# Kernel tuning notes

Measured on AMD Instinct MI355X. Metric: run time of the kernel, lower is better.

## Reference

```python
import jax, jax.numpy as jnp
import numpy as np

N = 100000        # nodes
E = 1600000       # edges (before self-loops)
F_IN = 128        # input feature dim
HID = 32          # hidden_channels
HEADS = 2
HC = HID * HEADS  # 64, per-conv output width (concat=True)
OUT = 40          # out_channels
NEG_SLOPE = 0.2   # PyG GATConv leaky_relu slope
BN_EPS = 1e-5


def setup_inputs() -> dict:
    key = jax.random.key(0)
    ks = jax.random.split(key, 16)
    g = lambda k, shape, s: jax.random.normal(k, shape, jnp.float32) * s
    node_feat = jax.random.normal(ks[0], (N, F_IN), jnp.float32)
    edge_index = jax.random.randint(ks[1], (2, E), 0, N, jnp.int32)
    inp = {
        "node_feat": node_feat,
        "edge_index": edge_index,
        "W1": g(ks[2], (F_IN, HC), 1.0 / np.sqrt(F_IN)),
        "a_src1": g(ks[3], (HEADS, HID), 0.1),
        "a_dst1": g(ks[4], (HEADS, HID), 0.1),
        "b1": jnp.zeros((HC,), jnp.float32),
        # BatchNorm1d(64) in eval mode (running stats)
        "bn_gamma": jnp.ones((HC,), jnp.float32),
        "bn_beta": jnp.zeros((HC,), jnp.float32),
        "bn_mean": g(ks[5], (HC,), 0.1),
        "bn_var": jax.random.uniform(ks[6], (HC,), jnp.float32, 0.5, 1.5),
        "W2": g(ks[7], (HC, HC), 1.0 / np.sqrt(HC)),
        "a_src2": g(ks[8], (HEADS, HID), 0.1),
        "a_dst2": g(ks[9], (HEADS, HID), 0.1),
        "b2": jnp.zeros((HC,), jnp.float32),
        # final projection 64 -> 40
        "Wf": g(ks[10], (HC, OUT), 1.0 / np.sqrt(HC)),
        "bf": jnp.zeros((OUT,), jnp.float32),
    }
    return inp


def _gat_layer(x, src, dst, W, a_s, a_d, b):
    # x: [N, Fin] -> h: [N, H, C]
    h = (x @ W).reshape(N, HEADS, HID)
    alpha_src = jnp.einsum('nhc,hc->nh', h, a_s)   # [N, H]
    alpha_dst = jnp.einsum('nhc,hc->nh', h, a_d)   # [N, H]
    e = jax.nn.leaky_relu(alpha_src[src] + alpha_dst[dst], NEG_SLOPE)  # [Etot, H]
    m = jax.lax.stop_gradient(jax.ops.segment_max(e, dst, num_segments=N))
    ex = jnp.exp(e - m[dst])
    denom = jax.ops.segment_sum(ex, dst, num_segments=N)
    alpha = ex / (denom[dst] + 1e-16)              # softmax over incoming edges
    msg = h[src] * alpha[:, :, None]               # [Etot, H, C]
    out = jax.ops.segment_sum(msg, dst, num_segments=N)  # [N, H, C]
    return out.reshape(N, HC) + b


def reference(node_feat, edge_index, W1, a_src1, a_dst1, b1,
              bn_gamma, bn_beta, bn_mean, bn_var,
              W2, a_src2, a_dst2, b2, Wf, bf):
    # add self-loops (PyG GATConv default add_self_loops=True)
    loop = jnp.arange(N, dtype=edge_index.dtype)
    src = jnp.concatenate([edge_index[0], loop])
    dst = jnp.concatenate([edge_index[1], loop])

    x1 = _gat_layer(node_feat, src, dst, W1, a_src1, a_dst1, b1)
    # BatchNorm1d eval + ELU (dropout is identity in eval)
    x1 = (x1 - bn_mean) * (bn_gamma / jnp.sqrt(bn_var + BN_EPS)) + bn_beta
    x1 = jax.nn.elu(x1)

    x2 = _gat_layer(x1, src, dst, W2, a_src2, a_dst2, b2)

    # JumpingKnowledge 'max': elementwise max over layer outputs
    xj = jnp.maximum(x1, x2)
    return xj @ Wf + bf
```

## Files before the change

### kernel.cpp

```cpp
#include <hip/hip_runtime.h>
#include <hip/hip_bf16.h>

#define N_NODES 100000
#define E_EDGES 1600000
#define ETOT    1700000
#define NB_SCAN 391
#define EQ4     400000
#define NB_EQ4  1563
#define F_IN    128
#define HC      64
#define OUT_C   40
#define NEG_SLOPE 0.2f
#define BN_EPS  1e-5f

#define P_W1   0
#define P_AS1  8192
#define P_AD1  8256
#define P_B1   8320
#define P_BNG  8384
#define P_BNB  8448
#define P_BNM  8512
#define P_BNV  8576
#define P_W2   8640
#define P_AS2  12736
#define P_AD2  12800
#define P_B2   12864
#define P_WF   12928
#define P_BF   15488
#define P_TOT  15528

typedef __attribute__((ext_vector_type(8))) short short8;
typedef __attribute__((ext_vector_type(4))) float floatx4;
typedef __attribute__((ext_vector_type(4))) unsigned int uintx4;

__device__ __forceinline__ unsigned short f2bf(float f) {
    unsigned int u = __float_as_uint(f);
    unsigned int r = u + 0x7FFFu + ((u >> 16) & 1u);
    return (unsigned short)(r >> 16);
}

__global__ __launch_bounds__(64) void detect_kernel(const unsigned short* __restrict__ x,
                                                    int* __restrict__ flag) {
    int t = threadIdx.x;
    bool huge = false;
#pragma unroll
    for (int i = 0; i < 4; ++i) {
        unsigned short u = x[(t * 4 + i) * 2];
        float v = __uint_as_float(((unsigned int)u) << 16);
        if (!(fabsf(v) < 1e4f)) huge = true;
    }
    unsigned long long b = __ballot(huge);
    if (t == 0) *flag = (b != 0ull) ? 1 : 0;
}

struct CvtArgs { const void* ptr[14]; int len[14]; };

__global__ __launch_bounds__(256) void cvt_params_kernel(CvtArgs a,
                                                         const int* __restrict__ flag,
                                                         float* __restrict__ dst) {
    int f = *flag;
    int i = blockIdx.x * 256 + threadIdx.x;
    if (i >= P_TOT) return;
    int k = 0, off = 0;
    while (i >= off + a.len[k]) { off += a.len[k]; ++k; }
    int j = i - off;
    float v = f ? ((const float*)a.ptr[k])[j]
                : __bfloat162float(((const __hip_bfloat16*)a.ptr[k])[j]);
    dst[i] = v;
}

__global__ __launch_bounds__(256) void build_frags_kernel(const float* __restrict__ prm,
                                                          unsigned short* __restrict__ fw1,
                                                          unsigned short* __restrict__ fw2) {
    int i = blockIdx.x * 256 + threadIdx.x;
    if (i < 8192) {
        int j = i & 7, l = (i >> 3) & 63, q = (i >> 9) & 3, t = i >> 11;
        int k = q * 32 + (l >> 4) * 8 + j;
        int n = t * 16 + (l & 15);
        fw1[i] = f2bf(prm[P_W1 + k * 64 + n]);
    } else if (i < 12288) {
        int f = i - 8192;
        int j = f & 7, l = (f >> 3) & 63, q = (f >> 9) & 1, t = f >> 10;
        int k = q * 32 + (l >> 4) * 8 + j;
        int n = t * 16 + (l & 15);
        fw2[f] = f2bf(prm[P_W2 + k * 64 + n]);
    }
}

__global__ __launch_bounds__(256) void histrank_kernel(const int* __restrict__ ei,
                                                       int* __restrict__ deg,
                                                       int4* __restrict__ rank4) {
    int i4 = blockIdx.x * 256 + threadIdx.x;
    if (i4 >= EQ4) return;
    const unsigned long long* dst2 = (const unsigned long long*)(ei + E_EDGES);
    unsigned long long p0 = __builtin_nontemporal_load(&dst2[i4 * 2]);
    unsigned long long p1 = __builtin_nontemporal_load(&dst2[i4 * 2 + 1]);
    int d0 = (int)(p0 & 0xFFFFFFFFull), d1 = (int)(p0 >> 32);
    int d2 = (int)(p1 & 0xFFFFFFFFull), d3 = (int)(p1 >> 32);
    int4 r;
    r.x = atomicAdd(&deg[d0], 1);
    r.y = atomicAdd(&deg[d1], 1);
    r.z = atomicAdd(&deg[d2], 1);
    r.w = atomicAdd(&deg[d3], 1);
    rank4[i4] = r;
}

__global__ __launch_bounds__(256) void scanA_kernel(const int* __restrict__ deg,
                                                    int* __restrict__ bsum) {
    __shared__ int sm[256];
    int t = threadIdx.x;
    int i = blockIdx.x * 256 + t;
    sm[t] = (i < N_NODES) ? deg[i] + 1 : 0;
    __syncthreads();
    for (int off = 128; off > 0; off >>= 1) {
        if (t < off) sm[t] += sm[t + off];
        __syncthreads();
    }
    if (t == 0) bsum[blockIdx.x] = sm[0];
}

__global__ __launch_bounds__(512) void scanB_kernel(const int* __restrict__ bsum,
                                                    int* __restrict__ boff,
                                                    int* __restrict__ row_start) {
    __shared__ int sm[512];
    int t = threadIdx.x;
    int v = (t < NB_SCAN) ? bsum[t] : 0;
    sm[t] = v;
    __syncthreads();
    for (int off = 1; off < 512; off <<= 1) {
        int o = (t >= off) ? sm[t - off] : 0;
        __syncthreads();
        sm[t] += o;
        __syncthreads();
    }
    if (t < NB_SCAN) boff[t] = sm[t] - v;
    if (t == NB_SCAN - 1) row_start[N_NODES] = sm[t];
}

__global__ __launch_bounds__(256) void scanC_kernel(const int* __restrict__ deg,
                                                    const int* __restrict__ boff,
                                                    int* __restrict__ row_start,
                                                    int* __restrict__ col) {
    __shared__ int sm[256];
    int t = threadIdx.x;
    int i = blockIdx.x * 256 + t;
    int v = (i < N_NODES) ? deg[i] + 1 : 0;
    sm[t] = v;
    __syncthreads();
    for (int off = 1; off < 256; off <<= 1) {
        int o = (t >= off) ? sm[t - off] : 0;
        __syncthreads();
        sm[t] += o;
        __syncthreads();
    }
    if (i < N_NODES) {
        int excl = sm[t] - v + boff[blockIdx.x];
        row_start[i] = excl;
        col[excl]    = i;
    }
}

__global__ __launch_bounds__(256) void scatter_kernel(const int* __restrict__ ei,
                                                      const int4* __restrict__ rank4,
                                                      const int* __restrict__ row_start,
                                                      int* __restrict__ col) {
    int i4 = blockIdx.x * 256 + threadIdx.x;
    if (i4 >= EQ4) return;
    const unsigned long long* dst2 = (const unsigned long long*)(ei + E_EDGES);
    const unsigned long long* src2 = (const unsigned long long*)ei;
    unsigned long long p0 = __builtin_nontemporal_load(&dst2[i4 * 2]);
    unsigned long long p1 = __builtin_nontemporal_load(&dst2[i4 * 2 + 1]);
    unsigned long long q0 = __builtin_nontemporal_load(&src2[i4 * 2]);
    unsigned long long q1 = __builtin_nontemporal_load(&src2[i4 * 2 + 1]);
    int4 r = rank4[i4];
    int d0 = (int)(p0 & 0xFFFFFFFFull), d1 = (int)(p0 >> 32);
    int d2 = (int)(p1 & 0xFFFFFFFFull), d3 = (int)(p1 >> 32);
    int s0 = (int)(q0 & 0xFFFFFFFFull), s1 = (int)(q0 >> 32);
    int s2 = (int)(q1 & 0xFFFFFFFFull), s3 = (int)(q1 >> 32);
    int b0 = row_start[d0];
    int b1 = row_start[d1];
    int b2 = row_start[d2];
    int b3 = row_start[d3];
    col[b0 + 1 + r.x] = s0;
    col[b1 + 1 + r.y] = s1;
    col[b2 + 1 + r.z] = s2;
    col[b3 + 1 + r.w] = s3;
}

__device__ __forceinline__ float leaky(float v) { return v > 0.f ? v : NEG_SLOPE * v; }

__device__ __forceinline__ float red64(float v) {
#pragma unroll
    for (int off = 32; off > 0; off >>= 1) v += __shfl_xor(v, off, 64);
    return v;
}
__device__ __forceinline__ float red16(float v) {
#pragma unroll
    for (int off = 8; off > 0; off >>= 1) v += __shfl_xor(v, off, 64);
    return v;
}

__global__ __launch_bounds__(128) void gemm1_kernel(const void* __restrict__ x,
                                                    const unsigned short* __restrict__ fw1,
                                                    const float* __restrict__ prm,
                                                    const int* __restrict__ flag,
                                                    unsigned short* __restrict__ h_bf,
                                                    float* __restrict__ as_,
                                                    float* __restrict__ ad_) {
    __shared__ short lx[2 * 4 * 64 * 8];
    int t = threadIdx.x;
    int f = *flag;
    int base = blockIdx.x * 32;

#pragma unroll
    for (int i = 0; i < 4; ++i) {
        int cid = i * 128 + t;
        int m = cid >> 4, c = cid & 15;
        int q = c >> 2, g = c & 3;
        int loff = (((m >> 4) * 4 + q) * 64 + g * 16 + (m & 15)) * 8;
        short8 s;
        if (f) {
            const float4* p = (const float4*)((const float*)x + ((size_t)(base + m) << 7) + (c << 3));
            float4 u0 = p[0], u1 = p[1];
            s[0] = (short)f2bf(u0.x); s[1] = (short)f2bf(u0.y);
            s[2] = (short)f2bf(u0.z); s[3] = (short)f2bf(u0.w);
            s[4] = (short)f2bf(u1.x); s[5] = (short)f2bf(u1.y);
            s[6] = (short)f2bf(u1.z); s[7] = (short)f2bf(u1.w);
        } else {
            s = *(const short8*)((const unsigned short*)x + ((size_t)(base + m) << 7) + (c << 3));
        }
        *(short8*)&lx[loff] = s;
    }
    __syncthreads();

    int w = t >> 6, lane = t & 63;
    short8 a[4];
#pragma unroll
    for (int q = 0; q < 4; ++q) a[q] = *(short8*)&lx[((w * 4 + q) * 64 + lane) * 8];

    const short8* bw = (const short8*)fw1;
    floatx4 acc[4];
#pragma unroll
    for (int tt = 0; tt < 4; ++tt) acc[tt] = (floatx4){0.f, 0.f, 0.f, 0.f};
#pragma unroll
    for (int tt = 0; tt < 4; ++tt) {
#pragma unroll
        for (int q = 0; q < 4; ++q) {
            short8 b = bw[(tt * 4 + q) * 64 + lane];
            acc[tt] = __builtin_amdgcn_mfma_f32_16x16x32_bf16(a[q], b, acc[tt], 0, 0, 0);
        }
    }

    int cl = lane & 15, grp = lane >> 4;
#pragma unroll
    for (int tt = 0; tt < 4; ++tt) {
#pragma unroll
        for (int r = 0; r < 4; ++r) {
            int node = base + w * 16 + grp * 4 + r;
            h_bf[(size_t)node * 64 + tt * 16 + cl] = f2bf(acc[tt][r]);
        }
    }

    float as0 = prm[P_AS1 + 0  + cl], as1 = prm[P_AS1 + 16 + cl],
          as2 = prm[P_AS1 + 32 + cl], as3 = prm[P_AS1 + 48 + cl];
    float ad0 = prm[P_AD1 + 0  + cl], ad1 = prm[P_AD1 + 16 + cl],
          ad2 = prm[P_AD1 + 32 + cl], ad3 = prm[P_AD1 + 48 + cl];
#pragma unroll
    for (int r = 0; r < 4; ++r) {
        float sh0 = red16(acc[0][r] * as0 + acc[1][r] * as1);
        float sh1 = red16(acc[2][r] * as2 + acc[3][r] * as3);
        float dh0 = red16(acc[0][r] * ad0 + acc[1][r] * ad1);
        float dh1 = red16(acc[2][r] * ad2 + acc[3][r] * ad3);
        if (cl == 0) {
            int node = base + w * 16 + grp * 4 + r;
            as_[node * 2] = sh0;  as_[node * 2 + 1] = sh1;
            ad_[node * 2] = dh0;  ad_[node * 2 + 1] = dh1;
        }
    }
}

__global__ __launch_bounds__(128) void gemm2_kernel(const unsigned short* __restrict__ x1_bf,
                                                    const unsigned short* __restrict__ fw2,
                                                    const float* __restrict__ prm,
                                                    unsigned short* __restrict__ h_bf,
                                                    float* __restrict__ as_,
                                                    float* __restrict__ ad_) {
    __shared__ short lx[2 * 2 * 64 * 8];
    int t = threadIdx.x;
    int base = blockIdx.x * 32;

#pragma unroll
    for (int i = 0; i < 2; ++i) {
        int cid = i * 128 + t;
        int m = cid >> 3, c = cid & 7;
        int q = c >> 2, g = c & 3;
        int loff = (((m >> 4) * 2 + q) * 64 + g * 16 + (m & 15)) * 8;
        short8 s = *(const short8*)(x1_bf + ((size_t)(base + m) << 6) + (c << 3));
        *(short8*)&lx[loff] = s;
    }
    __syncthreads();

    int w = t >> 6, lane = t & 63;
    short8 a[2];
#pragma unroll
    for (int q = 0; q < 2; ++q) a[q] = *(short8*)&lx[((w * 2 + q) * 64 + lane) * 8];

    const short8* bw = (const short8*)fw2;
    floatx4 acc[4];
#pragma unroll
    for (int tt = 0; tt < 4; ++tt) acc[tt] = (floatx4){0.f, 0.f, 0.f, 0.f};
#pragma unroll
    for (int tt = 0; tt < 4; ++tt) {
#pragma unroll
        for (int q = 0; q < 2; ++q) {
            short8 b = bw[(tt * 2 + q) * 64 + lane];
            acc[tt] = __builtin_amdgcn_mfma_f32_16x16x32_bf16(a[q], b, acc[tt], 0, 0, 0);
        }
    }

    int cl = lane & 15, grp = lane >> 4;
#pragma unroll
    for (int tt = 0; tt < 4; ++tt) {
#pragma unroll
        for (int r = 0; r < 4; ++r) {
            int node = base + w * 16 + grp * 4 + r;
            h_bf[(size_t)node * 64 + tt * 16 + cl] = f2bf(acc[tt][r]);
        }
    }

    float as0 = prm[P_AS2 + 0  + cl], as1 = prm[P_AS2 + 16 + cl],
          as2 = prm[P_AS2 + 32 + cl], as3 = prm[P_AS2 + 48 + cl];
    float ad0 = prm[P_AD2 + 0  + cl], ad1 = prm[P_AD2 + 16 + cl],
          ad2 = prm[P_AD2 + 32 + cl], ad3 = prm[P_AD2 + 48 + cl];
#pragma unroll
    for (int r = 0; r < 4; ++r) {
        float sh0 = red16(acc[0][r] * as0 + acc[1][r] * as1);
        float sh1 = red16(acc[2][r] * as2 + acc[3][r] * as3);
        float dh0 = red16(acc[0][r] * ad0 + acc[1][r] * ad1);
        float dh1 = red16(acc[2][r] * ad2 + acc[3][r] * ad3);
        if (cl == 0) {
            int node = base + w * 16 + grp * 4 + r;
            as_[node * 2] = sh0;  as_[node * 2 + 1] = sh1;
            ad_[node * 2] = dh0;  ad_[node * 2 + 1] = dh1;
        }
    }
}

__device__ __forceinline__ float slot_reduce(float acc[8], int lane) {
    int slot = lane & 7;
    bool b2 = (slot & 4) != 0;
#pragma unroll
    for (int q = 0; q < 4; ++q) {
        float send = b2 ? acc[q] : acc[q + 4];
        float recv = __shfl_xor(send, 4, 64);
        acc[q] = (b2 ? acc[q + 4] : acc[q]) + recv;
    }
    bool b1 = (slot & 2) != 0;
#pragma unroll
    for (int q = 0; q < 2; ++q) {
        float send = b1 ? acc[q] : acc[q + 2];
        float recv = __shfl_xor(send, 2, 64);
        acc[q] = (b1 ? acc[q + 2] : acc[q]) + recv;
    }
    bool b0 = (slot & 1) != 0;
    float send = b0 ? acc[0] : acc[1];
    float recv = __shfl_xor(send, 1, 64);
    return (b0 ? acc[1] : acc[0]) + recv;
}

template<int NK>
__device__ __forceinline__ void agg_rounds(const unsigned short* __restrict__ hb,
                                           const float* __restrict__ as_,
                                           const int* __restrict__ col,
                                           int rs, int koff, int last,
                                           int slot, int hi, float advh,
                                           float acc[8], float& sw) {
    int ce[NK]; float av[NK]; uintx4 dv[NK];
#pragma unroll
    for (int k = 0; k < NK; ++k) {
        int e = rs + koff + k * 8 + slot;
        ce[k] = col[e < last ? e : last];
    }
#pragma unroll
    for (int k = 0; k < NK; ++k)
        dv[k] = *(const uintx4*)(hb + ((size_t)ce[k] << 6));
#pragma unroll
    for (int k = 0; k < NK; ++k)
        av[k] = as_[ce[k] * 2 + hi];

    if constexpr (NK == 1) {
        asm volatile("" : "+v"(dv[0]), "+v"(av[0]));
    } else if constexpr (NK == 2) {
        asm volatile("" : "+v"(dv[0]), "+v"(dv[1]), "+v"(av[0]), "+v"(av[1]));
    } else if constexpr (NK == 3) {
        asm volatile("" : "+v"(dv[0]), "+v"(dv[1]), "+v"(dv[2]),
                          "+v"(av[0]), "+v"(av[1]), "+v"(av[2]));
    } else {
        asm volatile("" : "+v"(dv[0]), "+v"(dv[1]), "+v"(dv[2]), "+v"(dv[3]),
                          "+v"(av[0]), "+v"(av[1]), "+v"(av[2]), "+v"(av[3]));
    }

#pragma unroll
    for (int k = 0; k < NK; ++k) {
        int e = rs + koff + k * 8 + slot;
        float w = (e <= last) ? __expf(leaky(av[k] + advh)) : 0.f;
        sw += w;
#pragma unroll
        for (int q = 0; q < 4; ++q) {
            unsigned int dw = dv[k][q];
            acc[2 * q]     = fmaf(w, __uint_as_float(dw << 16),         acc[2 * q]);
            acc[2 * q + 1] = fmaf(w, __uint_as_float(dw & 0xFFFF0000u), acc[2 * q + 1]);
        }
    }
}

__device__ __forceinline__ float agg_core(const unsigned short* __restrict__ h_bf,
                                          const float* __restrict__ as_,
                                          const float* __restrict__ ad_,
                                          const int* __restrict__ col,
                                          int v, int rs, int re, int lane) {
    int deg  = re - rs;
    int slot = lane & 7;
    int cg   = lane >> 3;
    int hi   = cg >> 2;
    if (deg <= 64) {
        float advh = ad_[v * 2 + hi];
        const unsigned short* hb = h_bf + (cg << 3);
        int last = re - 1;
        float acc[8] = {0.f,0.f,0.f,0.f,0.f,0.f,0.f,0.f};
        float sw = 0.f;

        if (deg <= 8) {
            agg_rounds<1>(hb, as_, col, rs, 0, last, slot, hi, advh, acc, sw);
        } else if (deg <= 16) {
            agg_rounds<2>(hb, as_, col, rs, 0, last, slot, hi, advh, acc, sw);
        } else if (deg <= 24) {
            agg_rounds<3>(hb, as_, col, rs, 0, last, slot, hi, advh, acc, sw);
        } else {
            agg_rounds<4>(hb, as_, col, rs, 0, last, slot, hi, advh, acc, sw);
            if (deg > 32)
                agg_rounds<4>(hb, as_, col, rs, 32, last, slot, hi, advh, acc, sw);
        }

        sw += __shfl_xor(sw, 1, 64);
        sw += __shfl_xor(sw, 2, 64);
        sw += __shfl_xor(sw, 4, 64);
        float rdh = 1.f / (sw + 1e-16f);

        return slot_reduce(acc, lane) * rdh;
    } else {
        int head = lane >> 5;
        float adv0 = ad_[v * 2], adv1 = ad_[v * 2 + 1];
        float advh = head ? adv1 : adv0;
        float s0 = 0.f, s1 = 0.f;
        for (int e = rs + lane; e < re; e += 64) {
            int s = col[e];
            float2 av = *(const float2*)&as_[s * 2];
            s0 += __expf(leaky(av.x + adv0));
            s1 += __expf(leaky(av.y + adv1));
        }
        s0 = red64(s0); s1 = red64(s1);
        float rdh = 1.f / ((head ? s1 : s0) + 1e-16f);
        float a0 = 0.f;
        for (int e = rs; e < re; ++e) {
            int s = col[e];
            float w = __expf(leaky(as_[s * 2 + head] + advh));
            unsigned short u = h_bf[(size_t)s * 64 + lane];
            a0 = fmaf(w, __uint_as_float(((unsigned int)u) << 16), a0);
        }
        return a0 * rdh;
    }
}

__global__ __launch_bounds__(256, 6) void agg1_kernel(const unsigned short* __restrict__ h_bf,
                                                   const float* __restrict__ as_,
                                                   const float* __restrict__ ad_,
                                                   const int* __restrict__ row_start,
                                                   const int* __restrict__ col,
                                                   const float* __restrict__ bias,
                                                   const float* __restrict__ bn_g,
                                                   const float* __restrict__ bn_b,
                                                   const float* __restrict__ bn_m,
                                                   const float* __restrict__ bn_v,
                                                   unsigned short* __restrict__ x1_bf) {
    int t = threadIdx.x, wid = t >> 6, lane = t & 63;
    int v = blockIdx.x * 4 + wid;
    int rs = row_start[v], re = row_start[v + 1];
    float acc = agg_core(h_bf, as_, ad_, col, v, rs, re, lane);
    float r = acc + bias[lane];
    float scale = bn_g[lane] * rsqrtf(bn_v[lane] + BN_EPS);
    r = (r - bn_m[lane]) * scale + bn_b[lane];
    r = r > 0.f ? r : expm1f(r);
    x1_bf[(size_t)v * 64 + lane] = f2bf(r);
}

__global__ __launch_bounds__(256, 6) void agg2_kernel(const unsigned short* __restrict__ h_bf,
                                                   const float* __restrict__ as_,
                                                   const float* __restrict__ ad_,
                                                   const int* __restrict__ row_start,
                                                   const int* __restrict__ col,
                                                   const float* __restrict__ prm,
                                                   const unsigned short* __restrict__ x1_bf,
                                                   const int* __restrict__ flag,
                                                   void* __restrict__ out) {
    __shared__ float Wfs[2560];
    __shared__ float xsh[4][64];
    int t = threadIdx.x;
#pragma unroll
    for (int i = 0; i < 10; ++i) Wfs[i * 256 + t] = prm[P_WF + i * 256 + t];

    int wid = t >> 6, lane = t & 63;
    int v = blockIdx.x * 4 + wid;
    int rs = row_start[v], re = row_start[v + 1];
    float acc = agg_core(h_bf, as_, ad_, col, v, rs, re, lane);
    float x2 = acc + prm[P_B2 + lane];
    unsigned short u = x1_bf[(size_t)v * 64 + lane];
    float x1v = __uint_as_float(((unsigned int)u) << 16);
    xsh[wid][lane] = fmaxf(x1v, x2);
    __syncthreads();

    if (t < 160) {
        int n = t / 40, o = t - n * 40;
        float po = 0.f;
#pragma unroll
        for (int c = 0; c < 64; c += 4) {
            po = fmaf(xsh[n][c],     Wfs[c * 40 + o],       po);
            po = fmaf(xsh[n][c + 1], Wfs[(c + 1) * 40 + o], po);
            po = fmaf(xsh[n][c + 2], Wfs[(c + 2) * 40 + o], po);
            po = fmaf(xsh[n][c + 3], Wfs[(c + 3) * 40 + o], po);
        }
        float r = po + prm[P_BF + o];
        size_t idx = (size_t)(blockIdx.x * 4 + n) * 40 + o;
        if (*flag) ((float*)out)[idx] = r;
        else ((__hip_bfloat16*)out)[idx] = __float2bfloat16(r);
    }
}

extern "C" void kernel_launch(void* const* d_in, const int* in_sizes, int n_in,
                              void* d_out, int out_size, void* d_ws, size_t ws_size,
                              hipStream_t stream) {
    (void)in_sizes; (void)n_in; (void)out_size; (void)ws_size;
    const void* node_feat = d_in[0];
    const int*  edge_idx  = (const int*)d_in[1];

    char* ws = (char*)d_ws;
    size_t off = 0;
    auto alloc = [&](size_t bytes) -> void* {
        void* p = ws + off;
        off += (bytes + 255) & ~(size_t)255;
        return p;
    };
    unsigned short* h_bf  = (unsigned short*)alloc((size_t)N_NODES * 64 * 2);
    unsigned short* x1_bf = (unsigned short*)alloc((size_t)N_NODES * 64 * 2);
    float* as_ = (float*)alloc((size_t)N_NODES * 2 * 4);
    float* ad_ = (float*)alloc((size_t)N_NODES * 2 * 4);
    int* deg       = (int*)alloc((size_t)N_NODES * 4);
    int* row_start = (int*)alloc((size_t)(N_NODES + 1) * 4);
    int4* rank4    = (int4*)alloc((size_t)EQ4 * 16);
    int* col       = (int*)alloc((size_t)ETOT * 4);
    int* bsum      = (int*)alloc((size_t)NB_SCAN * 4);
    int* boff      = (int*)alloc((size_t)NB_SCAN * 4);
    float* prm     = (float*)alloc((size_t)P_TOT * 4);
    unsigned short* fw1 = (unsigned short*)alloc(8192 * 2);
    unsigned short* fw2 = (unsigned short*)alloc(4096 * 2);
    int* flag      = (int*)alloc(256);

    detect_kernel<<<1, 64, 0, stream>>>((const unsigned short*)node_feat, flag);
    CvtArgs ca;
    const int lens[14] = {8192, 64, 64, 64, 64, 64, 64, 64, 4096, 64, 64, 64, 2560, 40};
    for (int i = 0; i < 14; ++i) { ca.ptr[i] = d_in[i + 2]; ca.len[i] = lens[i]; }
    cvt_params_kernel<<<(P_TOT + 255) / 256, 256, 0, stream>>>(ca, flag, prm);
    build_frags_kernel<<<48, 256, 0, stream>>>(prm, fw1, fw2);

    hipMemsetAsync(deg, 0, (size_t)N_NODES * 4, stream);
    histrank_kernel<<<NB_EQ4, 256, 0, stream>>>(edge_idx, deg, rank4);
    scanA_kernel<<<NB_SCAN, 256, 0, stream>>>(deg, bsum);
    scanB_kernel<<<1, 512, 0, stream>>>(bsum, boff, row_start);
    scanC_kernel<<<NB_SCAN, 256, 0, stream>>>(deg, boff, row_start, col);
    scatter_kernel<<<NB_EQ4, 256, 0, stream>>>(edge_idx, rank4, row_start, col);

    gemm1_kernel<<<N_NODES / 32, 128, 0, stream>>>(node_feat, fw1, prm, flag,
                                                   h_bf, as_, ad_);
    agg1_kernel<<<N_NODES / 4, 256, 0, stream>>>(h_bf, as_, ad_, row_start, col,
                                                 prm + P_B1, prm + P_BNG, prm + P_BNB,
                                                 prm + P_BNM, prm + P_BNV, x1_bf);
    gemm2_kernel<<<N_NODES / 32, 128, 0, stream>>>(x1_bf, fw2, prm,
                                                   h_bf, as_, ad_);
    agg2_kernel<<<N_NODES / 4, 256, 0, stream>>>(h_bf, as_, ad_, row_start, col,
                                                 prm, x1_bf, flag, d_out);
}
```

Measured before the change: 380.4 us.

## Fuse degree histogram and layer-1 GEMM into one heterogeneous launch

Merges the atomic degree-histogram kernel and the first-layer MFMA GEMM into a single launch, with block index choosing the role. The two are independent, so the atomic-heavy histogram blocks and the compute/stream-bound GEMM blocks can overlap on the GPU, and one launch is removed. The GEMM part moves to 256-thread blocks covering 64 rows each, so the tail needs clamped loads and guarded stores. The histogram blocks now also reserve the larger shared-memory array, which may lower their occupancy.

```diff
diff --git a/kernel.cpp b/kernel.cpp
--- a/kernel.cpp
+++ b/kernel.cpp
@@ -7,6 +7,7 @@
 #define NB_SCAN 391
 #define EQ4     400000
 #define NB_EQ4  1563
+#define NGB     1563
 #define F_IN    128
 #define HC      64
 #define OUT_C   40
@@ -39,6 +40,19 @@
     return (unsigned short)(r >> 16);
 }
 
+__device__ __forceinline__ float leaky(float v) { return v > 0.f ? v : NEG_SLOPE * v; }
+
+__device__ __forceinline__ float red64(float v) {
+#pragma unroll
+    for (int off = 32; off > 0; off >>= 1) v += __shfl_xor(v, off, 64);
+    return v;
+}
+__device__ __forceinline__ float red16(float v) {
+#pragma unroll
+    for (int off = 8; off > 0; off >>= 1) v += __shfl_xor(v, off, 64);
+    return v;
+}
+
 __global__ __launch_bounds__(64) void detect_kernel(const unsigned short* __restrict__ x,
                                                     int* __restrict__ flag) {
     int t = threadIdx.x;
@@ -87,22 +101,101 @@
     }
 }
 
-__global__ __launch_bounds__(256) void histrank_kernel(const int* __restrict__ ei,
-                                                       int* __restrict__ deg,
-                                                       int4* __restrict__ rank4) {
-    int i4 = blockIdx.x * 256 + threadIdx.x;
-    if (i4 >= EQ4) return;
-    const unsigned long long* dst2 = (const unsigned long long*)(ei + E_EDGES);
-    unsigned long long p0 = __builtin_nontemporal_load(&dst2[i4 * 2]);
-    unsigned long long p1 = __builtin_nontemporal_load(&dst2[i4 * 2 + 1]);
-    int d0 = (int)(p0 & 0xFFFFFFFFull), d1 = (int)(p0 >> 32);
-    int d2 = (int)(p1 & 0xFFFFFFFFull), d3 = (int)(p1 >> 32);
-    int4 r;
-    r.x = atomicAdd(&deg[d0], 1);
-    r.y = atomicAdd(&deg[d1], 1);
-    r.z = atomicAdd(&deg[d2], 1);
-    r.w = atomicAdd(&deg[d3], 1);
-    rank4[i4] = r;
+__global__ __launch_bounds__(256) void fused_hist_gemm1_kernel(
+        const int* __restrict__ ei, int* __restrict__ deg, int4* __restrict__ rank4,
+        const void* __restrict__ x, const unsigned short* __restrict__ fw1,
+        const float* __restrict__ prm, const int* __restrict__ flag,
+        unsigned short* __restrict__ h_bf, float* __restrict__ as_,
+        float* __restrict__ ad_) {
+    __shared__ short lx[4 * 4 * 64 * 8];
+    if (blockIdx.x < NB_EQ4) {
+        int i4 = blockIdx.x * 256 + threadIdx.x;
+        if (i4 >= EQ4) return;
+        const unsigned long long* dst2 = (const unsigned long long*)(ei + E_EDGES);
+        unsigned long long p0 = __builtin_nontemporal_load(&dst2[i4 * 2]);
+        unsigned long long p1 = __builtin_nontemporal_load(&dst2[i4 * 2 + 1]);
+        int d0 = (int)(p0 & 0xFFFFFFFFull), d1 = (int)(p0 >> 32);
+        int d2 = (int)(p1 & 0xFFFFFFFFull), d3 = (int)(p1 >> 32);
+        int4 r;
+        r.x = atomicAdd(&deg[d0], 1);
+        r.y = atomicAdd(&deg[d1], 1);
+        r.z = atomicAdd(&deg[d2], 1);
+        r.w = atomicAdd(&deg[d3], 1);
+        rank4[i4] = r;
+        return;
+    }
+
+    int t = threadIdx.x;
+    int f = *flag;
+    int base = (blockIdx.x - NB_EQ4) * 64;
+
+#pragma unroll
+    for (int i = 0; i < 4; ++i) {
+        int cid = i * 256 + t;
+        int m = cid >> 4, c = cid & 15;
+        int q = c >> 2, g = c & 3;
+        int loff = (((m >> 4) * 4 + q) * 64 + g * 16 + (m & 15)) * 8;
+        int srow = base + m; if (srow > N_NODES - 1) srow = N_NODES - 1;
+        short8 s;
+        if (f) {
+            const float4* p = (const float4*)((const float*)x + ((size_t)srow << 7) + (c << 3));
+            float4 u0 = p[0], u1 = p[1];
+            s[0] = (short)f2bf(u0.x); s[1] = (short)f2bf(u0.y);
+            s[2] = (short)f2bf(u0.z); s[3] = (short)f2bf(u0.w);
+            s[4] = (short)f2bf(u1.x); s[5] = (short)f2bf(u1.y);
+            s[6] = (short)f2bf(u1.z); s[7] = (short)f2bf(u1.w);
+        } else {
+            s = *(const short8*)((const unsigned short*)x + ((size_t)srow << 7) + (c << 3));
+        }
+        *(short8*)&lx[loff] = s;
+    }
+    __syncthreads();
+
+    int w = t >> 6, lane = t & 63;
+    short8 a[4];
+#pragma unroll
+    for (int q = 0; q < 4; ++q) a[q] = *(short8*)&lx[((w * 4 + q) * 64 + lane) * 8];
+
+    const short8* bw = (const short8*)fw1;
+    floatx4 acc[4];
+#pragma unroll
+    for (int tt = 0; tt < 4; ++tt) acc[tt] = (floatx4){0.f, 0.f, 0.f, 0.f};
+#pragma unroll
+    for (int tt = 0; tt < 4; ++tt) {
+#pragma unroll
+        for (int q = 0; q < 4; ++q) {
+            short8 b = bw[(tt * 4 + q) * 64 + lane];
+            acc[tt] = __builtin_amdgcn_mfma_f32_16x16x32_bf16(a[q], b, acc[tt], 0, 0, 0);
+        }
+    }
+
+    int cl = lane & 15, grp = lane >> 4;
+#pragma unroll
+    for (int tt = 0; tt < 4; ++tt) {
+#pragma unroll
+        for (int r = 0; r < 4; ++r) {
+            int node = base + w * 16 + grp * 4 + r;
+            if (node < N_NODES)
+                h_bf[(size_t)node * 64 + tt * 16 + cl] = f2bf(acc[tt][r]);
+        }
+    }
+
+    float as0 = prm[P_AS1 + 0  + cl], as1 = prm[P_AS1 + 16 + cl],
+          as2 = prm[P_AS1 + 32 + cl], as3 = prm[P_AS1 + 48 + cl];
+    float ad0 = prm[P_AD1 + 0  + cl], ad1 = prm[P_AD1 + 16 + cl],
+          ad2 = prm[P_AD1 + 32 + cl], ad3 = prm[P_AD1 + 48 + cl];
+#pragma unroll
+    for (int r = 0; r < 4; ++r) {
+        float sh0 = red16(acc[0][r] * as0 + acc[1][r] * as1);
+        float sh1 = red16(acc[2][r] * as2 + acc[3][r] * as3);
+        float dh0 = red16(acc[0][r] * ad0 + acc[1][r] * ad1);
+        float dh1 = red16(acc[2][r] * ad2 + acc[3][r] * ad3);
+        int node = base + w * 16 + grp * 4 + r;
+        if (cl == 0 && node < N_NODES) {
+            as_[node * 2] = sh0;  as_[node * 2 + 1] = sh1;
+            ad_[node * 2] = dh0;  ad_[node * 2 + 1] = dh1;
+        }
+    }
 }
 
 __global__ __launch_bounds__(256) void scanA_kernel(const int* __restrict__ deg,
@@ -187,98 +280,6 @@
     col[b3 + 1 + r.w] = s3;
 }
 
-__device__ __forceinline__ float leaky(float v) { return v > 0.f ? v : NEG_SLOPE * v; }
-
-__device__ __forceinline__ float red64(float v) {
-#pragma unroll
-    for (int off = 32; off > 0; off >>= 1) v += __shfl_xor(v, off, 64);
-    return v;
-}
-__device__ __forceinline__ float red16(float v) {
-#pragma unroll
-    for (int off = 8; off > 0; off >>= 1) v += __shfl_xor(v, off, 64);
-    return v;
-}
-
-__global__ __launch_bounds__(128) void gemm1_kernel(const void* __restrict__ x,
-                                                    const unsigned short* __restrict__ fw1,
-                                                    const float* __restrict__ prm,
-                                                    const int* __restrict__ flag,
-                                                    unsigned short* __restrict__ h_bf,
-                                                    float* __restrict__ as_,
-                                                    float* __restrict__ ad_) {
-    __shared__ short lx[2 * 4 * 64 * 8];
-    int t = threadIdx.x;
-    int f = *flag;
-    int base = blockIdx.x * 32;
-
-#pragma unroll
-    for (int i = 0; i < 4; ++i) {
-        int cid = i * 128 + t;
-        int m = cid >> 4, c = cid & 15;
-        int q = c >> 2, g = c & 3;
-        int loff = (((m >> 4) * 4 + q) * 64 + g * 16 + (m & 15)) * 8;
-        short8 s;
-        if (f) {
-            const float4* p = (const float4*)((const float*)x + ((size_t)(base + m) << 7) + (c << 3));
-            float4 u0 = p[0], u1 = p[1];
-            s[0] = (short)f2bf(u0.x); s[1] = (short)f2bf(u0.y);
-            s[2] = (short)f2bf(u0.z); s[3] = (short)f2bf(u0.w);
-            s[4] = (short)f2bf(u1.x); s[5] = (short)f2bf(u1.y);
-            s[6] = (short)f2bf(u1.z); s[7] = (short)f2bf(u1.w);
-        } else {
-            s = *(const short8*)((const unsigned short*)x + ((size_t)(base + m) << 7) + (c << 3));
-        }
-        *(short8*)&lx[loff] = s;
-    }
-    __syncthreads();
-
-    int w = t >> 6, lane = t & 63;
-    short8 a[4];
-#pragma unroll
-    for (int q = 0; q < 4; ++q) a[q] = *(short8*)&lx[((w * 4 + q) * 64 + lane) * 8];
-
-    const short8* bw = (const short8*)fw1;
-    floatx4 acc[4];
-#pragma unroll
-    for (int tt = 0; tt < 4; ++tt) acc[tt] = (floatx4){0.f, 0.f, 0.f, 0.f};
-#pragma unroll
-    for (int tt = 0; tt < 4; ++tt) {
-#pragma unroll
-        for (int q = 0; q < 4; ++q) {
-            short8 b = bw[(tt * 4 + q) * 64 + lane];
-            acc[tt] = __builtin_amdgcn_mfma_f32_16x16x32_bf16(a[q], b, acc[tt], 0, 0, 0);
-        }
-    }
-
-    int cl = lane & 15, grp = lane >> 4;
-#pragma unroll
-    for (int tt = 0; tt < 4; ++tt) {
-#pragma unroll
-        for (int r = 0; r < 4; ++r) {
-            int node = base + w * 16 + grp * 4 + r;
-            h_bf[(size_t)node * 64 + tt * 16 + cl] = f2bf(acc[tt][r]);
-        }
-    }
-
-    float as0 = prm[P_AS1 + 0  + cl], as1 = prm[P_AS1 + 16 + cl],
-          as2 = prm[P_AS1 + 32 + cl], as3 = prm[P_AS1 + 48 + cl];
-    float ad0 = prm[P_AD1 + 0  + cl], ad1 = prm[P_AD1 + 16 + cl],
-          ad2 = prm[P_AD1 + 32 + cl], ad3 = prm[P_AD1 + 48 + cl];
-#pragma unroll
-    for (int r = 0; r < 4; ++r) {
-        float sh0 = red16(acc[0][r] * as0 + acc[1][r] * as1);
-        float sh1 = red16(acc[2][r] * as2 + acc[3][r] * as3);
-        float dh0 = red16(acc[0][r] * ad0 + acc[1][r] * ad1);
-        float dh1 = red16(acc[2][r] * ad2 + acc[3][r] * ad3);
-        if (cl == 0) {
-            int node = base + w * 16 + grp * 4 + r;
-            as_[node * 2] = sh0;  as_[node * 2 + 1] = sh1;
-            ad_[node * 2] = dh0;  ad_[node * 2 + 1] = dh1;
-        }
-    }
-}
-
 __global__ __launch_bounds__(128) void gemm2_kernel(const unsigned short* __restrict__ x1_bf,
                                                     const unsigned short* __restrict__ fw2,
                                                     const float* __restrict__ prm,
@@ -573,14 +574,13 @@
     build_frags_kernel<<<48, 256, 0, stream>>>(prm, fw1, fw2);
 
     hipMemsetAsync(deg, 0, (size_t)N_NODES * 4, stream);
-    histrank_kernel<<<NB_EQ4, 256, 0, stream>>>(edge_idx, deg, rank4);
+    fused_hist_gemm1_kernel<<<NB_EQ4 + NGB, 256, 0, stream>>>(
+        edge_idx, deg, rank4, node_feat, fw1, prm, flag, h_bf, as_, ad_);
     scanA_kernel<<<NB_SCAN, 256, 0, stream>>>(deg, bsum);
     scanB_kernel<<<1, 512, 0, stream>>>(bsum, boff, row_start);
     scanC_kernel<<<NB_SCAN, 256, 0, stream>>>(deg, boff, row_start, col);
     scatter_kernel<<<NB_EQ4, 256, 0, stream>>>(edge_idx, rank4, row_start, col);
 
-    gemm1_kernel<<<N_NODES / 32, 128, 0, stream>>>(node_feat, fw1, prm, flag,
-                                                   h_bf, as_, ad_);
     agg1_kernel<<<N_NODES / 4, 256, 0, stream>>>(h_bf, as_, ad_, row_start, col,
                                                  prm + P_B1, prm + P_BNG, prm + P_BNB,
                                                  prm + P_BNM, prm + P_BNV, x1_bf);
```

Result: faster. 371.3 us (-2.4%).
